# Optimization experiments

Measured on AMD Instinct MI355X. Metric: run time of the kernel, lower is better.

## Reference

```python
import jax, jax.numpy as jnp
import numpy as np

N_NODES = 50000
N_EDGES = 800000
IN_DIM = 128
NUM_HEADS = 8
OUT_DIM = 16  # per-head dim; NUM_HEADS*OUT_DIM == IN_DIM


def setup_inputs() -> dict:
    key = jax.random.key(0)
    ks = jax.random.split(key, 9)
    s = 1.0 / np.sqrt(IN_DIM)
    return {
        "h": jax.random.normal(ks[0], (N_NODES, IN_DIM), dtype=jnp.float32),
        "src": jax.random.randint(ks[1], (N_EDGES,), 0, N_NODES),
        "dst": jax.random.randint(ks[2], (N_EDGES,), 0, N_NODES),
        "WQ": jax.random.normal(ks[3], (IN_DIM, NUM_HEADS * OUT_DIM), dtype=jnp.float32) * s,
        "bQ": jnp.zeros((NUM_HEADS * OUT_DIM,), dtype=jnp.float32),
        "WK": jax.random.normal(ks[4], (IN_DIM, NUM_HEADS * OUT_DIM), dtype=jnp.float32) * s,
        "bK": jnp.zeros((NUM_HEADS * OUT_DIM,), dtype=jnp.float32),
        "WV": jax.random.normal(ks[5], (IN_DIM, NUM_HEADS * OUT_DIM), dtype=jnp.float32) * s,
        "bV": jnp.zeros((NUM_HEADS * OUT_DIM,), dtype=jnp.float32),
    }


def reference(h, src, dst, WQ, bQ, WK, bK, WV, bV):
    N = h.shape[0]
    # node projections -> [N, H, D]
    Q = (h @ WQ + bQ).reshape(N, NUM_HEADS, OUT_DIM)
    K = (h @ WK + bK).reshape(N, NUM_HEADS, OUT_DIM)
    V = (h @ WV + bV).reshape(N, NUM_HEADS, OUT_DIM)
    # edge-wise score: (K_src * Q_dst) summed over D, scaled by sqrt(D)
    inv_scale = 1.0 / np.sqrt(OUT_DIM)
    score = jnp.einsum("ehd,ehd->eh", K[src], Q[dst]) * inv_scale  # [E, H]
    score_soft = jnp.exp(jnp.clip(score, -5.0, 5.0))[..., None]    # [E, H, 1]
    # scatter-sum messages to destination nodes
    wV = jax.ops.segment_sum(V[src] * score_soft, dst, num_segments=N)  # [N, H, D]
    z = jax.ops.segment_sum(score_soft, dst, num_segments=N)            # [N, H, 1]
    return wV / (z + 1e-6)
```

## Files before the change

kernel.cpp:

```cpp
#include <hip/hip_runtime.h>
#include <hip/hip_bf16.h>

#define IN_DIM 128
#define NUM_HEADS 8
#define OUT_DIM 16

#define BKT_SHIFT 7
#define BKT_MASK 127
#define NB_MAX 512
#define SLAB_SHIFT 13

typedef unsigned int uint;
typedef unsigned short ushort;
using short8 = __attribute__((ext_vector_type(8))) short;
using f32x4  = __attribute__((ext_vector_type(4))) float;
using u32x2  = __attribute__((ext_vector_type(2))) uint;

__device__ inline uint cvt_pk_bf16(float a, float b) {
    uint r;
    asm("v_cvt_pk_bf16_f32 %0, %1, %2" : "=v"(r) : "v"(a), "v"(b));
    return r;
}

__global__ __launch_bounds__(256) void stage_wtrans(const int* __restrict__ src,
                                                    const int* __restrict__ dst,
                                                    int* __restrict__ bucketCursor,
                                                    uint* __restrict__ slab,
                                                    const float* __restrict__ WQ,
                                                    const float* __restrict__ WK,
                                                    const float* __restrict__ WV,
                                                    ushort* __restrict__ WT,
                                                    int nEdges, int nb, int sb) {
    const int t = threadIdx.x;

    if ((int)blockIdx.x >= sb) {
        int tid = (blockIdx.x - sb) * 256 + t;
        if (tid >= 384 * 16) return;
        int n = tid >> 4;
        int kg = tid & 15;
        const float* W = (n < 128) ? WQ : (n < 256) ? WK : WV;
        int c = n & 127;
        union { short8 s; uint u[4]; } o;
        #pragma unroll
        for (int j = 0; j < 4; ++j) {
            float v0 = W[(kg * 8 + 2 * j) * 128 + c];
            float v1 = W[(kg * 8 + 2 * j + 1) * 128 + c];
            o.u[j] = cvt_pk_bf16(v0, v1);
        }
        *(short8*)(WT + (size_t)n * 128 + kg * 8) = o.s;
        return;
    }

    __shared__ int cnt[4][NB_MAX];
    __shared__ int base[4][NB_MAX];
    const int wv = t >> 6;
    const int e0 = blockIdx.x * 2048;

    for (int i = t; i < 4 * NB_MAX; i += 256) ((int*)cnt)[i] = 0;
    __syncthreads();

    int myDst[8], mySrc[8];
    #pragma unroll
    for (int i = 0; i < 2; ++i) {
        int e = e0 + (i * 256 + t) * 4;
        if (e + 3 < nEdges) {
            int4 d4 = *(const int4*)(dst + e);
            int4 s4 = *(const int4*)(src + e);
            myDst[4*i+0] = d4.x; myDst[4*i+1] = d4.y; myDst[4*i+2] = d4.z; myDst[4*i+3] = d4.w;
            mySrc[4*i+0] = s4.x; mySrc[4*i+1] = s4.y; mySrc[4*i+2] = s4.z; mySrc[4*i+3] = s4.w;
        } else {
            #pragma unroll
            for (int k = 0; k < 4; ++k) {
                int ee = e + k;
                myDst[4*i+k] = (ee < nEdges) ? dst[ee] : -1;
                mySrc[4*i+k] = (ee < nEdges) ? src[ee] : 0;
            }
        }
    }
    #pragma unroll
    for (int i = 0; i < 8; ++i)
        if (myDst[i] >= 0) atomicAdd(&cnt[wv][myDst[i] >> BKT_SHIFT], 1);
    __syncthreads();

    for (int bb = t; bb < NB_MAX; bb += 256) {
        int c0 = cnt[0][bb], c1 = cnt[1][bb], c2 = cnt[2][bb], c3 = cnt[3][bb];
        int tot = c0 + c1 + c2 + c3;
        int gbase = (bb < nb && tot > 0) ? atomicAdd(&bucketCursor[bb], tot) : 0;
        base[0][bb] = gbase;
        base[1][bb] = gbase + c0;
        base[2][bb] = gbase + c0 + c1;
        base[3][bb] = gbase + c0 + c1 + c2;
    }
    __syncthreads();
    for (int i = t; i < 4 * NB_MAX; i += 256) ((int*)cnt)[i] = 0;
    __syncthreads();

    #pragma unroll
    for (int i = 0; i < 8; ++i) {
        int d = myDst[i];
        if (d >= 0) {
            int b = d >> BKT_SHIFT;
            int pos = base[wv][b] + atomicAdd(&cnt[wv][b], 1);
            if (pos < (1 << SLAB_SHIFT))
                slab[((size_t)b << SLAB_SHIFT) + pos] = (uint)mySrc[i] | ((uint)(d & BKT_MASK) << 17);
        }
    }
}

__global__ __launch_bounds__(64, 2) void sort_proj(const uint* __restrict__ slab,
                                                   const int* __restrict__ bucketCursor,
                                                   int* __restrict__ offsets,
                                                   int* __restrict__ srcSorted,
                                                   const float* __restrict__ h,
                                                   const short* __restrict__ WT,
                                                   const float* __restrict__ bQ,
                                                   const float* __restrict__ bK,
                                                   const float* __restrict__ bV,
                                                   uint* __restrict__ Qout,
                                                   uint* __restrict__ KVout,
                                                   int nNodes, int nEdges, int nb) {
    const int t = threadIdx.x;

    if ((int)blockIdx.x < nb) {
        __shared__ int cnt[128];
        __shared__ int sOutBase;
        const int b = blockIdx.x;
        const int count = bucketCursor[b];
        const uint* rec = slab + ((size_t)b << SLAB_SHIFT);

        int acc = 0;
        for (int i = t; i < b; i += 64) acc += bucketCursor[i];
        #pragma unroll
        for (int off = 32; off; off >>= 1) acc += __shfl_down(acc, off);
        if (t == 0) sOutBase = acc;
        cnt[t] = 0; cnt[t + 64] = 0;
        __syncthreads();

        for (int i = t; i < count; i += 64)
            atomicAdd(&cnt[rec[i] >> 17], 1);
        __syncthreads();

        const int outBase = sOutBase;
        int c0 = cnt[2 * t], c1 = cnt[2 * t + 1];
        int s = c0 + c1;
        int x = s;
        #pragma unroll
        for (int off = 1; off < 64; off <<= 1) { int y = __shfl_up(x, off); if (t >= off) x += y; }
        int prefix = x - s;
        int node0 = b << BKT_SHIFT;
        int g0 = node0 + 2 * t, g1 = node0 + 2 * t + 1;
        if (g0 < nNodes) offsets[g0] = outBase + prefix;
        if (g1 < nNodes) offsets[g1] = outBase + prefix + c0;
        __syncthreads();
        cnt[2 * t] = prefix;
        cnt[2 * t + 1] = prefix + c0;
        __syncthreads();

        for (int i = t; i < count; i += 64) {
            uint r = rec[i];
            int pos = atomicAdd(&cnt[r >> 17], 1);
            srcSorted[outBase + pos] = (int)(r & 0x1ffff);
        }
        if (b == 0 && t == 0) offsets[nNodes] = nEdges;
        return;
    }

    const int gw = blockIdx.x - nb;
    const int lane = t;
    const int lr = lane & 15;
    const int q = lane >> 4;
    const int node0 = (gw >> 1) * 64;
    const int chalf = gw & 1;

    short8 a[4][4];
    #pragma unroll
    for (int g = 0; g < 4; ++g) {
        const int row = node0 + g * 16 + lr;
        const bool ok = row < nNodes;
        #pragma unroll
        for (int ks = 0; ks < 4; ++ks) {
            union { short8 s; uint u[4]; } v;
            if (ok) {
                const float* p = h + (size_t)row * 128 + (ks * 4 + q) * 8;
                float4 f0 = *(const float4*)p;
                float4 f1 = *(const float4*)(p + 4);
                v.u[0] = cvt_pk_bf16(f0.x, f0.y);
                v.u[1] = cvt_pk_bf16(f0.z, f0.w);
                v.u[2] = cvt_pk_bf16(f1.x, f1.y);
                v.u[3] = cvt_pk_bf16(f1.z, f1.w);
            } else {
                v.s = (short8)0;
            }
            a[g][ks] = v.s;
        }
    }

    const short8* WT8 = (const short8*)WT;

    #pragma unroll 1
    for (int cc = 0; cc < 4; ++cc) {
        const int c = chalf * 4 + cc;
        const int nq = c * 16 + lr;
        f32x4 aQ[4] = {{0,0,0,0},{0,0,0,0},{0,0,0,0},{0,0,0,0}};
        f32x4 aK[4] = {{0,0,0,0},{0,0,0,0},{0,0,0,0},{0,0,0,0}};
        f32x4 aV[4] = {{0,0,0,0},{0,0,0,0},{0,0,0,0},{0,0,0,0}};
        #pragma unroll
        for (int ks = 0; ks < 4; ++ks) {
            short8 bq = WT8[(size_t)nq * 16 + ks * 4 + q];
            short8 bk = WT8[(size_t)(nq + 128) * 16 + ks * 4 + q];
            short8 bv = WT8[(size_t)(nq + 256) * 16 + ks * 4 + q];
            #pragma unroll
            for (int g = 0; g < 4; ++g) {
                aQ[g] = __builtin_amdgcn_mfma_f32_16x16x32_bf16(a[g][ks], bq, aQ[g], 0, 0, 0);
                aK[g] = __builtin_amdgcn_mfma_f32_16x16x32_bf16(a[g][ks], bk, aK[g], 0, 0, 0);
                aV[g] = __builtin_amdgcn_mfma_f32_16x16x32_bf16(a[g][ks], bv, aV[g], 0, 0, 0);
            }
        }
        const float biasq = bQ[nq];
        const float biask = bK[nq];
        const float biasv = bV[nq];
        #pragma unroll
        for (int g = 0; g < 4; ++g) {
            #pragma unroll
            for (int r = 0; r < 4; ++r) {
                int node = node0 + g * 16 + q * 4 + r;
                float qval = aQ[g][r] + biasq;
                float qpart = __shfl_xor(qval, 1);
                if (node < nNodes) {
                    if ((lr & 1) == 0)
                        Qout[(size_t)node * 64 + (nq >> 1)] = cvt_pk_bf16(qval, qpart);
                    KVout[(size_t)node * 128 + nq] = cvt_pk_bf16(aK[g][r] + biask, aV[g][r] + biasv);
                }
            }
        }
    }
}

__global__ __launch_bounds__(256) void agg_kernel(const int* __restrict__ offsets,
                                                  const int* __restrict__ srcSorted,
                                                  const uint* __restrict__ Q,
                                                  const uint4* __restrict__ KV,
                                                  float* __restrict__ out,
                                                  int nNodes) {
    int wid = (int)((blockIdx.x * (size_t)blockDim.x + threadIdx.x) >> 6);
    if (wid >= nNodes) return;
    const int lane = threadIdx.x & 63;
    const int li = lane & 31;
    const int hf = lane >> 5;
    const int beg = offsets[wid];
    const int end = offsets[wid + 1];

    u32x2 qp = __builtin_nontemporal_load((const u32x2*)(Q + (size_t)wid * 64) + li);
    f32x4 qv;
    qv.x = __uint_as_float(qp.x << 16);
    qv.y = __uint_as_float(qp.x & 0xffff0000u);
    qv.z = __uint_as_float(qp.y << 16);
    qv.w = __uint_as_float(qp.y & 0xffff0000u);

    f32x4 acc = {0.f, 0.f, 0.f, 0.f};
    float zacc = 0.f;

    auto compute = [&](uint4 u, float mask) {
        float k0 = __uint_as_float(u.x << 16), v0 = __uint_as_float(u.x & 0xffff0000u);
        float k1 = __uint_as_float(u.y << 16), v1 = __uint_as_float(u.y & 0xffff0000u);
        float k2 = __uint_as_float(u.z << 16), v2 = __uint_as_float(u.z & 0xffff0000u);
        float k3 = __uint_as_float(u.w << 16), v3 = __uint_as_float(u.w & 0xffff0000u);
        float p = k0 * qv.x + k1 * qv.y + k2 * qv.z + k3 * qv.w;
        p += __shfl_xor(p, 1);
        p += __shfl_xor(p, 2);
        float e = __expf(fminf(fmaxf(p * 0.25f, -5.0f), 5.0f)) * mask;
        acc.x += v0 * e; acc.y += v1 * e; acc.z += v2 * e; acc.w += v3 * e;
        zacc += e;
    };

    int j = beg;
    for (; j + 8 <= end; j += 8) {
        int sI[4];
        #pragma unroll
        for (int i = 0; i < 4; ++i) sI[i] = __builtin_nontemporal_load(srcSorted + j + 2 * i + hf);
        uint4 u[4];
        #pragma unroll
        for (int i = 0; i < 4; ++i) u[i] = KV[(size_t)sI[i] * 32 + li];
        #pragma unroll
        for (int i = 0; i < 4; ++i) compute(u[i], 1.f);
    }
    for (; j + 2 <= end; j += 2) {
        uint4 u = KV[(size_t)srcSorted[j + hf] * 32 + li];
        compute(u, 1.f);
    }
    if (j < end) {
        uint4 u = KV[(size_t)srcSorted[j] * 32 + li];
        compute(u, hf ? 0.f : 1.f);
    }

    acc.x += __shfl_xor(acc.x, 32);
    acc.y += __shfl_xor(acc.y, 32);
    acc.z += __shfl_xor(acc.z, 32);
    acc.w += __shfl_xor(acc.w, 32);
    zacc  += __shfl_xor(zacc, 32);

    if (hf == 0) {
        float inv = 1.0f / (zacc + 1e-6f);
        f32x4 o = {acc.x * inv, acc.y * inv, acc.z * inv, acc.w * inv};
        __builtin_nontemporal_store(o, (f32x4*)(out + (size_t)wid * 128) + li);
    }
}

extern "C" void kernel_launch(void* const* d_in, const int* in_sizes, int n_in,
                              void* d_out, int out_size, void* d_ws, size_t ws_size,
                              hipStream_t stream) {
    const float* h   = (const float*)d_in[0];
    const int*   src = (const int*)d_in[1];
    const int*   dst = (const int*)d_in[2];
    const float* WQ  = (const float*)d_in[3];
    const float* bQ  = (const float*)d_in[4];
    const float* WK  = (const float*)d_in[5];
    const float* bK  = (const float*)d_in[6];
    const float* WV  = (const float*)d_in[7];
    const float* bV  = (const float*)d_in[8];

    const int nNodes = in_sizes[0] / IN_DIM;
    const int nEdges = in_sizes[1];
    const int nb = (nNodes + (1 << BKT_SHIFT) - 1) >> BKT_SHIFT;

    float* out = (float*)d_out;
    const size_t nf = (size_t)nNodes * 128;

    uint*   Qw          = (uint*)d_ws;
    uint*   KVw         = Qw + (size_t)nNodes * 64;
    ushort* WTw         = (ushort*)(KVw + nf);
    int*    bucketCursor= (int*)(WTw + 384 * 128);
    int*    offsets     = bucketCursor + NB_MAX;
    int*    srcSorted   = offsets + (nNodes + 1);
    uint*   slab        = (uint*)(srcSorted + nEdges);

    (void)hipMemsetAsync(bucketCursor, 0, NB_MAX * sizeof(int), stream);

    int sb = (nEdges + 2047) / 2048;
    stage_wtrans<<<sb + 24, 256, 0, stream>>>(src, dst, bucketCursor, slab,
                                              WQ, WK, WV, WTw, nEdges, nb, sb);

    int projWaves = ((nNodes + 63) / 64) * 2;
    sort_proj<<<nb + projWaves, 64, 0, stream>>>(slab, bucketCursor, offsets, srcSorted,
                                                 h, (const short*)WTw, bQ, bK, bV,
                                                 Qw, KVw, nNodes, nEdges, nb);

    int aggBlocks = (nNodes * 64 + 255) / 256;
    agg_kernel<<<aggBlocks, 256, 0, stream>>>(offsets, srcSorted, Qw, (const uint4*)KVw, out, nNodes);
}
```

Before: 118.3 us.

## Regroup stages: prep weights, co-schedule projection with edge bucketing, widen sort blocks

The kernel pipeline is regrouped. A small prep kernel now transposes the weights and zeroes the bucket cursors, replacing the memset. The projection GEMM moves into the same launch as edge bucketing, with projection and bucketing blocks interleaved so the compute-heavy and memory/atomic-heavy work overlap. The bucket sort becomes its own kernel with 256-thread blocks instead of 64, which adds a launch but gives the per-bucket counting and scatter more parallelism.

```diff
diff --git a/kernel.cpp b/kernel.cpp
--- a/kernel.cpp
+++ b/kernel.cpp
@@ -22,39 +22,131 @@
     return r;
 }
 
-__global__ __launch_bounds__(256) void stage_wtrans(const int* __restrict__ src,
-                                                    const int* __restrict__ dst,
-                                                    int* __restrict__ bucketCursor,
-                                                    uint* __restrict__ slab,
-                                                    const float* __restrict__ WQ,
-                                                    const float* __restrict__ WK,
-                                                    const float* __restrict__ WV,
-                                                    ushort* __restrict__ WT,
-                                                    int nEdges, int nb, int sb) {
+__global__ __launch_bounds__(256) void prep_kernel(const float* __restrict__ WQ,
+                                                   const float* __restrict__ WK,
+                                                   const float* __restrict__ WV,
+                                                   ushort* __restrict__ WT,
+                                                   int* __restrict__ bucketCursor) {
     const int t = threadIdx.x;
-
-    if ((int)blockIdx.x >= sb) {
-        int tid = (blockIdx.x - sb) * 256 + t;
-        if (tid >= 384 * 16) return;
-        int n = tid >> 4;
-        int kg = tid & 15;
-        const float* W = (n < 128) ? WQ : (n < 256) ? WK : WV;
-        int c = n & 127;
-        union { short8 s; uint u[4]; } o;
-        #pragma unroll
-        for (int j = 0; j < 4; ++j) {
-            float v0 = W[(kg * 8 + 2 * j) * 128 + c];
-            float v1 = W[(kg * 8 + 2 * j + 1) * 128 + c];
-            o.u[j] = cvt_pk_bf16(v0, v1);
-        }
-        *(short8*)(WT + (size_t)n * 128 + kg * 8) = o.s;
+    if (blockIdx.x == 24) {
+        for (int i = t; i < NB_MAX; i += 256) bucketCursor[i] = 0;
         return;
     }
-
+    int tid = blockIdx.x * 256 + t;
+    int n = tid >> 4;
+    int kg = tid & 15;
+    const float* W = (n < 128) ? WQ : (n < 256) ? WK : WV;
+    int c = n & 127;
+    union { short8 s; uint u[4]; } o;
+    #pragma unroll
+    for (int j = 0; j < 4; ++j) {
+        float v0 = W[(kg * 8 + 2 * j) * 128 + c];
+        float v1 = W[(kg * 8 + 2 * j + 1) * 128 + c];
+        o.u[j] = cvt_pk_bf16(v0, v1);
+    }
+    *(short8*)(WT + (size_t)n * 128 + kg * 8) = o.s;
+}
+
+__global__ __launch_bounds__(256, 2) void proj_stage(const float* __restrict__ h,
+                                                     const short* __restrict__ WT,
+                                                     const float* __restrict__ bQ,
+                                                     const float* __restrict__ bK,
+                                                     const float* __restrict__ bV,
+                                                     uint* __restrict__ Qout,
+                                                     uint* __restrict__ KVout,
+                                                     const int* __restrict__ src,
+                                                     const int* __restrict__ dst,
+                                                     int* __restrict__ bucketCursor,
+                                                     uint* __restrict__ slab,
+                                                     int nNodes, int nEdges, int nb,
+                                                     int projBlocks, int sb) {
     __shared__ int cnt[4][NB_MAX];
     __shared__ int base[4][NB_MAX];
+    const int t = threadIdx.x;
+
+    const int nMin = (projBlocks < sb) ? projBlocks : sb;
+    int bid = blockIdx.x;
+    bool isProj;
+    int idx;
+    if (bid < 2 * nMin) { isProj = !(bid & 1); idx = bid >> 1; }
+    else { idx = bid - 2 * nMin + nMin; isProj = (projBlocks > sb); }
+
+    if (isProj) {
+        const int lane = t & 63;
+        const int gw = idx * 4 + (t >> 6);
+        const int lr = lane & 15;
+        const int q = lane >> 4;
+        const int node0 = (gw >> 1) * 64;
+        const int chalf = gw & 1;
+        if (node0 >= nNodes) return;
+
+        short8 a[4][4];
+        #pragma unroll
+        for (int g = 0; g < 4; ++g) {
+            const int row = node0 + g * 16 + lr;
+            const bool ok = row < nNodes;
+            #pragma unroll
+            for (int ks = 0; ks < 4; ++ks) {
+                union { short8 s; uint u[4]; } v;
+                if (ok) {
+                    const float* p = h + (size_t)row * 128 + (ks * 4 + q) * 8;
+                    float4 f0 = *(const float4*)p;
+                    float4 f1 = *(const float4*)(p + 4);
+                    v.u[0] = cvt_pk_bf16(f0.x, f0.y);
+                    v.u[1] = cvt_pk_bf16(f0.z, f0.w);
+                    v.u[2] = cvt_pk_bf16(f1.x, f1.y);
+                    v.u[3] = cvt_pk_bf16(f1.z, f1.w);
+                } else {
+                    v.s = (short8)0;
+                }
+                a[g][ks] = v.s;
+            }
+        }
+
+        const short8* WT8 = (const short8*)WT;
+
+        #pragma unroll 1
+        for (int cc = 0; cc < 4; ++cc) {
+            const int c = chalf * 4 + cc;
+            const int nq = c * 16 + lr;
+            f32x4 aQ[4] = {{0,0,0,0},{0,0,0,0},{0,0,0,0},{0,0,0,0}};
+            f32x4 aK[4] = {{0,0,0,0},{0,0,0,0},{0,0,0,0},{0,0,0,0}};
+            f32x4 aV[4] = {{0,0,0,0},{0,0,0,0},{0,0,0,0},{0,0,0,0}};
+            #pragma unroll
+            for (int ks = 0; ks < 4; ++ks) {
+                short8 bq = WT8[(size_t)nq * 16 + ks * 4 + q];
+                short8 bk = WT8[(size_t)(nq + 128) * 16 + ks * 4 + q];
+                short8 bv = WT8[(size_t)(nq + 256) * 16 + ks * 4 + q];
+                #pragma unroll
+                for (int g = 0; g < 4; ++g) {
+                    aQ[g] = __builtin_amdgcn_mfma_f32_16x16x32_bf16(a[g][ks], bq, aQ[g], 0, 0, 0);
+                    aK[g] = __builtin_amdgcn_mfma_f32_16x16x32_bf16(a[g][ks], bk, aK[g], 0, 0, 0);
+                    aV[g] = __builtin_amdgcn_mfma_f32_16x16x32_bf16(a[g][ks], bv, aV[g], 0, 0, 0);
+                }
+            }
+            const float biasq = bQ[nq];
+            const float biask = bK[nq];
+            const float biasv = bV[nq];
+            #pragma unroll
+            for (int g = 0; g < 4; ++g) {
+                #pragma unroll
+                for (int r = 0; r < 4; ++r) {
+                    int node = node0 + g * 16 + q * 4 + r;
+                    float qval = aQ[g][r] + biasq;
+                    float qpart = __shfl_xor(qval, 1);
+                    if (node < nNodes) {
+                        if ((lr & 1) == 0)
+                            Qout[(size_t)node * 64 + (nq >> 1)] = cvt_pk_bf16(qval, qpart);
+                        KVout[(size_t)node * 128 + nq] = cvt_pk_bf16(aK[g][r] + biask, aV[g][r] + biasv);
+                    }
+                }
+            }
+        }
+        return;
+    }
+
     const int wv = t >> 6;
-    const int e0 = blockIdx.x * 2048;
+    const int e0 = idx * 2048;
 
     for (int i = t; i < 4 * NB_MAX; i += 256) ((int*)cnt)[i] = 0;
     __syncthreads();
@@ -107,40 +199,35 @@
     }
 }
 
-__global__ __launch_bounds__(64, 2) void sort_proj(const uint* __restrict__ slab,
+__global__ __launch_bounds__(256) void bucket_sort(const uint* __restrict__ slab,
                                                    const int* __restrict__ bucketCursor,
                                                    int* __restrict__ offsets,
                                                    int* __restrict__ srcSorted,
-                                                   const float* __restrict__ h,
-                                                   const short* __restrict__ WT,
-                                                   const float* __restrict__ bQ,
-                                                   const float* __restrict__ bK,
-                                                   const float* __restrict__ bV,
-                                                   uint* __restrict__ Qout,
-                                                   uint* __restrict__ KVout,
                                                    int nNodes, int nEdges, int nb) {
+    __shared__ int cnt[128];
+    __shared__ int sOutBase;
+    const int b = blockIdx.x;
     const int t = threadIdx.x;
-
-    if ((int)blockIdx.x < nb) {
-        __shared__ int cnt[128];
-        __shared__ int sOutBase;
-        const int b = blockIdx.x;
-        const int count = bucketCursor[b];
-        const uint* rec = slab + ((size_t)b << SLAB_SHIFT);
-
+    const int count = bucketCursor[b];
+    const uint* rec = slab + ((size_t)b << SLAB_SHIFT);
+
+    if (t < 128) cnt[t] = 0;
+    if (t >= 64 && t < 128) {
+        int l = t - 64;
         int acc = 0;
-        for (int i = t; i < b; i += 64) acc += bucketCursor[i];
+        for (int i = l; i < b; i += 64) acc += bucketCursor[i];
         #pragma unroll
         for (int off = 32; off; off >>= 1) acc += __shfl_down(acc, off);
-        if (t == 0) sOutBase = acc;
-        cnt[t] = 0; cnt[t + 64] = 0;
-        __syncthreads();
-
-        for (int i = t; i < count; i += 64)
-            atomicAdd(&cnt[rec[i] >> 17], 1);
-        __syncthreads();
-
-        const int outBase = sOutBase;
+        if (l == 0) sOutBase = acc;
+    }
+    __syncthreads();
+
+    for (int i = t; i < count; i += 256)
+        atomicAdd(&cnt[rec[i] >> 17], 1);
+    __syncthreads();
+
+    const int outBase = sOutBase;
+    if (t < 64) {
         int c0 = cnt[2 * t], c1 = cnt[2 * t + 1];
         int s = c0 + c1;
         int x = s;
@@ -151,89 +238,17 @@
         int g0 = node0 + 2 * t, g1 = node0 + 2 * t + 1;
         if (g0 < nNodes) offsets[g0] = outBase + prefix;
         if (g1 < nNodes) offsets[g1] = outBase + prefix + c0;
-        __syncthreads();
         cnt[2 * t] = prefix;
         cnt[2 * t + 1] = prefix + c0;
-        __syncthreads();
-
-        for (int i = t; i < count; i += 64) {
-            uint r = rec[i];
-            int pos = atomicAdd(&cnt[r >> 17], 1);
-            srcSorted[outBase + pos] = (int)(r & 0x1ffff);
-        }
-        if (b == 0 && t == 0) offsets[nNodes] = nEdges;
-        return;
-    }
-
-    const int gw = blockIdx.x - nb;
-    const int lane = t;
-    const int lr = lane & 15;
-    const int q = lane >> 4;
-    const int node0 = (gw >> 1) * 64;
-    const int chalf = gw & 1;
-
-    short8 a[4][4];
-    #pragma unroll
-    for (int g = 0; g < 4; ++g) {
-        const int row = node0 + g * 16 + lr;
-        const bool ok = row < nNodes;
-        #pragma unroll
-        for (int ks = 0; ks < 4; ++ks) {
-            union { short8 s; uint u[4]; } v;
-            if (ok) {
-                const float* p = h + (size_t)row * 128 + (ks * 4 + q) * 8;
-                float4 f0 = *(const float4*)p;
-                float4 f1 = *(const float4*)(p + 4);
-                v.u[0] = cvt_pk_bf16(f0.x, f0.y);
-                v.u[1] = cvt_pk_bf16(f0.z, f0.w);
-                v.u[2] = cvt_pk_bf16(f1.x, f1.y);
-                v.u[3] = cvt_pk_bf16(f1.z, f1.w);
-            } else {
-                v.s = (short8)0;
-            }
-            a[g][ks] = v.s;
-        }
-    }
-
-    const short8* WT8 = (const short8*)WT;
-
-    #pragma unroll 1
-    for (int cc = 0; cc < 4; ++cc) {
-        const int c = chalf * 4 + cc;
-        const int nq = c * 16 + lr;
-        f32x4 aQ[4] = {{0,0,0,0},{0,0,0,0},{0,0,0,0},{0,0,0,0}};
-        f32x4 aK[4] = {{0,0,0,0},{0,0,0,0},{0,0,0,0},{0,0,0,0}};
-        f32x4 aV[4] = {{0,0,0,0},{0,0,0,0},{0,0,0,0},{0,0,0,0}};
-        #pragma unroll
-        for (int ks = 0; ks < 4; ++ks) {
-            short8 bq = WT8[(size_t)nq * 16 + ks * 4 + q];
-            short8 bk = WT8[(size_t)(nq + 128) * 16 + ks * 4 + q];
-            short8 bv = WT8[(size_t)(nq + 256) * 16 + ks * 4 + q];
-            #pragma unroll
-            for (int g = 0; g < 4; ++g) {
-                aQ[g] = __builtin_amdgcn_mfma_f32_16x16x32_bf16(a[g][ks], bq, aQ[g], 0, 0, 0);
-                aK[g] = __builtin_amdgcn_mfma_f32_16x16x32_bf16(a[g][ks], bk, aK[g], 0, 0, 0);
-                aV[g] = __builtin_amdgcn_mfma_f32_16x16x32_bf16(a[g][ks], bv, aV[g], 0, 0, 0);
-            }
-        }
-        const float biasq = bQ[nq];
-        const float biask = bK[nq];
-        const float biasv = bV[nq];
-        #pragma unroll
-        for (int g = 0; g < 4; ++g) {
-            #pragma unroll
-            for (int r = 0; r < 4; ++r) {
-                int node = node0 + g * 16 + q * 4 + r;
-                float qval = aQ[g][r] + biasq;
-                float qpart = __shfl_xor(qval, 1);
-                if (node < nNodes) {
-                    if ((lr & 1) == 0)
-                        Qout[(size_t)node * 64 + (nq >> 1)] = cvt_pk_bf16(qval, qpart);
-                    KVout[(size_t)node * 128 + nq] = cvt_pk_bf16(aK[g][r] + biask, aV[g][r] + biasv);
-                }
-            }
-        }
-    }
+    }
+    __syncthreads();
+
+    for (int i = t; i < count; i += 256) {
+        uint r = rec[i];
+        int pos = atomicAdd(&cnt[r >> 17], 1);
+        srcSorted[outBase + pos] = (int)(r & 0x1ffff);
+    }
+    if (b == 0 && t == 0) offsets[nNodes] = nEdges;
 }
 
 __global__ __launch_bounds__(256) void agg_kernel(const int* __restrict__ offsets,
@@ -334,16 +349,16 @@
     int*    srcSorted   = offsets + (nNodes + 1);
     uint*   slab        = (uint*)(srcSorted + nEdges);
 
-    (void)hipMemsetAsync(bucketCursor, 0, NB_MAX * sizeof(int), stream);
-
+    prep_kernel<<<25, 256, 0, stream>>>(WQ, WK, WV, WTw, bucketCursor);
+
+    int projWaveUnits = ((nNodes + 63) / 64) * 2;
+    int projBlocks = (projWaveUnits + 3) / 4;
     int sb = (nEdges + 2047) / 2048;
-    stage_wtrans<<<sb + 24, 256, 0, stream>>>(src, dst, bucketCursor, slab,
-                                              WQ, WK, WV, WTw, nEdges, nb, sb);
-
-    int projWaves = ((nNodes + 63) / 64) * 2;
-    sort_proj<<<nb + projWaves, 64, 0, stream>>>(slab, bucketCursor, offsets, srcSorted,
-                                                 h, (const short*)WTw, bQ, bK, bV,
-                                                 Qw, KVw, nNodes, nEdges, nb);
+    proj_stage<<<projBlocks + sb, 256, 0, stream>>>(h, (const short*)WTw, bQ, bK, bV,
+                                                    Qw, KVw, src, dst, bucketCursor, slab,
+                                                    nNodes, nEdges, nb, projBlocks, sb);
+
+    bucket_sort<<<nb, 256, 0, stream>>>(slab, bucketCursor, offsets, srcSorted, nNodes, nEdges, nb);
 
     int aggBlocks = (nNodes * 64 + 255) / 256;
     agg_kernel<<<aggBlocks, 256, 0, stream>>>(offsets, srcSorted, Qw, (const uint4*)KVw, out, nNodes);
```

After: 133.8 us. 1.13x slower.
